# Kernel optimization log

Measured on AMD Instinct MI355X. Metric: run time of the kernel, lower is better.

The kernel has to match this reference:

```python
import jax, jax.numpy as jnp
import numpy as np

EMBED_DIM = 1024
HEAD = 16
DK = EMBED_DIM // HEAD  # 64
B, S = 2, 2048
NEG = -1.0e9


def setup_inputs() -> dict:
    key = jax.random.key(0)
    ks = jax.random.split(key, 8)
    d = {
        'query': jax.random.normal(ks[0], (B, S, EMBED_DIM), jnp.float32),
        'key': jax.random.normal(ks[1], (B, S, EMBED_DIM), jnp.float32),
        'value': jax.random.normal(ks[2], (B, S, EMBED_DIM), jnp.float32),
        'masked': jax.random.randint(ks[3], (B, S, S), 0, 2).astype(bool),
        'Wq': jax.random.normal(ks[4], (EMBED_DIM, EMBED_DIM), jnp.float32) / np.sqrt(EMBED_DIM),
        'Wk': jax.random.normal(ks[5], (EMBED_DIM, EMBED_DIM), jnp.float32) / np.sqrt(EMBED_DIM),
        'Wv': jax.random.normal(ks[6], (EMBED_DIM, EMBED_DIM), jnp.float32) / np.sqrt(EMBED_DIM),
        'Wo': jax.random.normal(ks[7], (EMBED_DIM, EMBED_DIM), jnp.float32) / np.sqrt(EMBED_DIM),
    }
    return d


def reference(query, key, value, masked, Wq, Wk, Wv, Wo):
    # projections (bias-free Linear: x @ W), split into heads: [B, H, S, DK]
    def split_heads(x):
        b, s, _ = x.shape
        return x.reshape(b, s, HEAD, DK).transpose(0, 2, 1, 3)

    q = split_heads(query @ Wq)
    k = split_heads(key @ Wk)
    v = split_heads(value @ Wv)

    scale = 1.0 / jnp.sqrt(jnp.asarray(DK, q.dtype))
    scores = jnp.einsum('bhqd,bhkd->bhqk', q, k) * scale
    scores = jnp.where(masked[:, None, :, :], NEG, scores)
    attn = jax.nn.softmax(scores, axis=-1)
    out = jnp.einsum('bhqk,bhkd->bhqd', attn, v)  # [B, H, S, DK]
    out = out.transpose(0, 2, 1, 3).reshape(query.shape[0], -1, EMBED_DIM)
    return out @ Wo
```

## Files before the change

kernel.cpp:

```cpp
#include <hip/hip_runtime.h>
#include <hip/hip_bf16.h>

typedef float f32x4 __attribute__((ext_vector_type(4)));
typedef __bf16 bf16x8 __attribute__((ext_vector_type(8)));
typedef _Float16 f16x2 __attribute__((ext_vector_type(2)));
typedef _Float16 f16x4 __attribute__((ext_vector_type(4)));

__device__ __forceinline__ unsigned short f2bf(float f){
  unsigned int u = __builtin_bit_cast(unsigned int, f);
  u += 0x7fffu + ((u >> 16) & 1u);
  return (unsigned short)(u >> 16);
}
__device__ __forceinline__ float bf2f(unsigned short h){
  return __builtin_bit_cast(float, (unsigned int)h << 16);
}

__device__ __forceinline__ f16x2 pkrtz(float a, float b){
  return __builtin_bit_cast(f16x2, __builtin_amdgcn_cvt_pkrtz(a, b));
}

__device__ __forceinline__ void glds16(const void* g, void* l){
  __builtin_amdgcn_global_load_lds((const __attribute__((address_space(1))) void*)g,
                                   (__attribute__((address_space(3))) void*)l, 16, 0, 0);
}

__device__ __forceinline__ f32x4 mfma16(bf16x8 a, bf16x8 b, f32x4 c){
  return __builtin_amdgcn_mfma_f32_16x16x32_bf16(a, b, c, 0, 0, 0);
}
__device__ __forceinline__ f32x4 mfma16h(f16x4 a, f16x4 b, f32x4 c){
  return __builtin_amdgcn_mfma_f32_16x16x16f16(a, b, c, 0, 0, 0);
}

#if __has_builtin(__builtin_amdgcn_exp2f)
__device__ __forceinline__ float exp2v(float x){ return __builtin_amdgcn_exp2f(x); }
#else
__device__ __forceinline__ float exp2v(float x){ return exp2f(x); }
#endif

__global__ void detect_kernel(const unsigned int* __restrict__ m, int* __restrict__ flag){
  int t = threadIdx.x;
  int bad = 0;
  for(int i = t; i < 4096; i += 256) bad |= (m[i] > 1u);
  unsigned long long b = __ballot(bad != 0);
  __shared__ int sbuf[4];
  if((t & 63) == 0) sbuf[t >> 6] = (b != 0ull);
  __syncthreads();
  if(t == 0) flag[0] = (sbuf[0] | sbuf[1] | sbuf[2] | sbuf[3]) ? 0 : 1;
}

__global__ void pack_mask_kernel(const unsigned char* __restrict__ m8,
                                 unsigned int* __restrict__ mp,
                                 const int* __restrict__ flag){
  const int wid = threadIdx.x >> 6, lane = threadIdx.x & 63;
  const int row = blockIdx.x * 4 + wid;
  const int is32 = flag[0];
  const int* m32 = (const int*)m8;
  for(int c0 = 0; c0 < 2048; c0 += 64){
    int mv = is32 ? m32[(size_t)row*2048 + c0 + lane]
                  : (int)m8[(size_t)row*2048 + c0 + lane];
    unsigned long long b = __ballot(mv != 0);
    if(lane == 0){
      mp[(size_t)row*64 + (c0 >> 5)]     = (unsigned int)b;
      mp[(size_t)row*64 + (c0 >> 5) + 1] = (unsigned int)(b >> 32);
    }
  }
}

__global__ void cvt3_kernel(const float* __restrict__ qs, const float* __restrict__ ks,
                            const float* __restrict__ vs, unsigned short* __restrict__ dst){
  const float* src = (blockIdx.y==0)?qs:(blockIdx.y==1)?ks:vs;
  unsigned short* d = dst + (size_t)blockIdx.y * 4194304;
  int i = blockIdx.x * 256 + threadIdx.x;
  const float4* s = (const float4*)src;
  float4 a = s[2*i], b = s[2*i+1];
  union { unsigned short h[8]; uint4 v; } o;
  o.h[0]=f2bf(a.x); o.h[1]=f2bf(a.y); o.h[2]=f2bf(a.z); o.h[3]=f2bf(a.w);
  o.h[4]=f2bf(b.x); o.h[5]=f2bf(b.y); o.h[6]=f2bf(b.z); o.h[7]=f2bf(b.w);
  ((uint4*)d)[i] = o.v;
}

__global__ void transW_kernel(const float* __restrict__ Wq, const float* __restrict__ Wk,
                              const float* __restrict__ Wv, const float* __restrict__ Wo,
                              unsigned short* __restrict__ WT){
  const float* W = (blockIdx.y==0)?Wq:(blockIdx.y==1)?Wk:(blockIdx.y==2)?Wv:Wo;
  const float scale = (blockIdx.y==0) ? 0.1803368801111601f : 1.0f;
  unsigned short* D = WT + (size_t)blockIdx.y * 1048576;
  int r0 = (blockIdx.x >> 4) * 64, c0 = (blockIdx.x & 15) * 64;
  __shared__ unsigned short T[64][65];
  int t = threadIdx.x;
  {
    int r = t >> 2, cb = (t & 3) * 16;
    const float4* src = (const float4*)(W + (size_t)(r0 + r) * 1024 + (c0 + cb));
    float4 v0 = src[0], v1 = src[1], v2 = src[2], v3 = src[3];
    float vals[16] = {v0.x,v0.y,v0.z,v0.w, v1.x,v1.y,v1.z,v1.w,
                      v2.x,v2.y,v2.z,v2.w, v3.x,v3.y,v3.z,v3.w};
    #pragma unroll
    for(int j=0;j<16;j++) T[cb + j][r] = f2bf(vals[j] * scale);
  }
  __syncthreads();
  {
    int c = t >> 2, rb = (t & 3) * 16;
    union { unsigned short h[16]; uint4 v[2]; } o;
    #pragma unroll
    for(int j=0;j<16;j++) o.h[j] = T[c][rb + j];
    uint4* dp = (uint4*)(D + (size_t)(c0 + c) * 1024 + (r0 + rb));
    dp[0] = o.v[0]; dp[1] = o.v[1];
  }
}

template<int OUTF32>
__global__ __launch_bounds__(256,2) void gemm_bt(
    const unsigned short* __restrict__ A0, const unsigned short* __restrict__ A1, const unsigned short* __restrict__ A2,
    const unsigned short* __restrict__ B0, const unsigned short* __restrict__ B1, const unsigned short* __restrict__ B2,
    unsigned short* __restrict__ C0, unsigned short* __restrict__ C1, unsigned short* __restrict__ C2,
    float* __restrict__ Cf)
{
  const unsigned short* A  = (blockIdx.z==0)?A0:(blockIdx.z==1)?A1:A2;
  const unsigned short* BT = (blockIdx.z==0)?B0:(blockIdx.z==1)?B1:B2;
  unsigned short* C        = (blockIdx.z==0)?C0:(blockIdx.z==1)?C1:C2;
  __shared__ unsigned short Asm[128*64];
  __shared__ unsigned short Bsm[128*64];
  const int wid = threadIdx.x >> 6, lane = threadIdx.x & 63;
  const int m0 = blockIdx.x * 128, n0 = blockIdx.y * 128;
  const int wrow = wid >> 1, wcol = wid & 1;
  const int li = lane & 15, lg = lane >> 4, li7 = lane & 7;
  f32x4 acc[4][4] = {};
  const int sr = lane >> 3;
  const int sc = lane & 7;

  for(int kt = 0; kt < 16; ++kt){
    const int kofs = kt * 64;
    #pragma unroll
    for(int i=0;i<4;i++){
      int r = wid*32 + i*8 + sr;
      int blk = sc ^ sr;
      glds16(A  + (size_t)(m0 + r)*1024 + kofs + blk*8, &Asm[(wid*32 + i*8)*64]);
      glds16(BT + (size_t)(n0 + r)*1024 + kofs + blk*8, &Bsm[(wid*32 + i*8)*64]);
    }
    __syncthreads();
    #pragma unroll
    for(int kk=0; kk<2; kk++){
      bf16x8 af[4], bfv[4];
      #pragma unroll
      for(int fm=0; fm<4; fm++){
        int row = wrow*64 + fm*16 + li;
        int blk = (kk*4 + lg) ^ li7;
        af[fm] = *(const bf16x8*)&Asm[row*64 + blk*8];
      }
      #pragma unroll
      for(int fn=0; fn<4; fn++){
        int row = wcol*64 + fn*16 + li;
        int blk = (kk*4 + lg) ^ li7;
        bfv[fn] = *(const bf16x8*)&Bsm[row*64 + blk*8];
      }
      __builtin_amdgcn_s_setprio(1);
      #pragma unroll
      for(int fm=0; fm<4; fm++)
        #pragma unroll
        for(int fn=0; fn<4; fn++)
          acc[fm][fn] = mfma16(af[fm], bfv[fn], acc[fm][fn]);
      __builtin_amdgcn_s_setprio(0);
    }
    __syncthreads();
  }
  if(OUTF32 == 0 && blockIdx.z == 2){
    #pragma unroll
    for(int fm=0; fm<4; fm++){
      #pragma unroll
      for(int fn=0; fn<4; fn++){
        int col  = n0 + wcol*64 + fn*16 + li;
        int rowb = m0 + wrow*64 + fm*16 + lg*4;
        int bq = rowb >> 11, s = rowb & 2047;
        union { f16x2 h2[2]; unsigned long long u; } o;
        o.h2[0] = pkrtz(acc[fm][fn][0], acc[fm][fn][1]);
        o.h2[1] = pkrtz(acc[fm][fn][2], acc[fm][fn][3]);
        *(unsigned long long*)&C[((size_t)(bq*16 + (col>>6))*64 + (col&63))*2048 + s] = o.u;
      }
    }
  } else {
    #pragma unroll
    for(int fm=0; fm<4; fm++){
      #pragma unroll
      for(int fn=0; fn<4; fn++){
        int col  = n0 + wcol*64 + fn*16 + li;
        int rowb = m0 + wrow*64 + fm*16 + lg*4;
        #pragma unroll
        for(int r=0;r<4;r++){
          if(OUTF32) Cf[(size_t)(rowb + r)*1024 + col] = acc[fm][fn][r];
          else       C [(size_t)(rowb + r)*1024 + col] = f2bf(acc[fm][fn][r]);
        }
      }
    }
  }
}

__global__ __launch_bounds__(256,2) void attn_kernel(
    const unsigned short* __restrict__ Q, const unsigned short* __restrict__ K,
    const unsigned short* __restrict__ Vt, unsigned short* __restrict__ O,
    const unsigned int* __restrict__ mp)
{
  __shared__ unsigned short Ksm[2][64*64];
  __shared__ unsigned short Vsm[2][64*64];
  const int wid = threadIdx.x >> 6, lane = threadIdx.x & 63;
  const int orig = blockIdx.x;
  const int wg = (orig & 7) * 64 + (orig >> 3);
  const int qt = wg & 15, bh = wg >> 4;
  const int b = bh >> 4, h = bh & 15;
  const int q0 = qt * 128;
  const int li = lane & 15, lg = lane >> 4;
  const int li7 = li & 7;

  const int rowA = b*2048 + q0 + wid*32 + li;
  const int rowB = rowA + 16;

  bf16x8 qfA[2], qfB[2];
  {
    const unsigned short* qa = Q + (size_t)rowA*1024 + h*64 + lg*8;
    const unsigned short* qb = Q + (size_t)rowB*1024 + h*64 + lg*8;
    qfA[0] = *(const bf16x8*)qa; qfA[1] = *(const bf16x8*)(qa + 32);
    qfB[0] = *(const bf16x8*)qb; qfB[1] = *(const bf16x8*)(qb + 32);
  }

  f32x4 oaccA[4] = {}, oaccB[4] = {};
  float lrowA = 0.f, lrowB = 0.f;

  const int srow = lane >> 3;
  const int sblk = (lane & 7) ^ srow;

  #pragma unroll
  for(int i=0;i<2;i++){
    int r = wid*16 + i*8 + srow;
    glds16(K  + (size_t)(b*2048 + r)*1024 + h*64 + sblk*8, &Ksm[0][(wid*16 + i*8)*64]);
    glds16(Vt + (size_t)(bh*64 + r)*2048 + sblk*8,         &Vsm[0][(wid*16 + i*8)*64]);
  }
  uint2 mwA = *(const uint2*)&mp[(size_t)rowA*64];
  uint2 mwB = *(const uint2*)&mp[(size_t)rowB*64];
  uint2 mwAn, mwBn;
  __syncthreads();

  int buf = 0;
  for(int t = 0; t < 32; ++t){
    const int kv0 = t * 64;
    if(t < 31){
      #pragma unroll
      for(int i=0;i<2;i++){
        int r = wid*16 + i*8 + srow;
        glds16(K  + (size_t)(b*2048 + kv0 + 64 + r)*1024 + h*64 + sblk*8, &Ksm[buf^1][(wid*16 + i*8)*64]);
        glds16(Vt + (size_t)(bh*64 + r)*2048 + kv0 + 64 + sblk*8,         &Vsm[buf^1][(wid*16 + i*8)*64]);
      }
      mwAn = *(const uint2*)&mp[(size_t)rowA*64 + (size_t)((kv0 + 64) >> 5)];
      mwBn = *(const uint2*)&mp[(size_t)rowB*64 + (size_t)((kv0 + 64) >> 5)];
    }
    f32x4 pA[4], pB[4];
    __builtin_amdgcn_s_setprio(1);
    #pragma unroll
    for(int f=0; f<4; f++){
      f32x4 sa = {0.f,0.f,0.f,0.f}, sb = {0.f,0.f,0.f,0.f};
      #pragma unroll
      for(int kf=0; kf<2; kf++){
        int blk = (kf*4 + lg) ^ li7;
        bf16x8 kfr = *(const bf16x8*)&Ksm[buf][(f*16 + li)*64 + blk*8];
        sa = mfma16(kfr, qfA[kf], sa);
        sb = mfma16(kfr, qfB[kf], sb);
      }
      pA[f] = sa; pB[f] = sb;
    }
    __builtin_amdgcn_s_setprio(0);
    #pragma unroll
    for(int f=0; f<4; f++){
      unsigned int wA = (f < 2) ? mwA.x : mwA.y;
      unsigned int wB = (f < 2) ? mwB.x : mwB.y;
      float eA[4], eB[4];
      #pragma unroll
      for(int j=0;j<4;j++){
        unsigned int bitA = (wA >> ((f & 1)*16 + lg*4 + j)) & 1u;
        unsigned int bitB = (wB >> ((f & 1)*16 + lg*4 + j)) & 1u;
        float vA = exp2v(pA[f][j]);
        float vB = exp2v(pB[f][j]);
        eA[j] = bitA ? 0.f : vA;
        eB[j] = bitB ? 0.f : vB;
      }
      lrowA += (eA[0] + eA[1]) + (eA[2] + eA[3]);
      lrowB += (eB[0] + eB[1]) + (eB[2] + eB[3]);
      union { f16x2 h2[2]; f16x4 v; } ua, ub;
      ua.h2[0] = pkrtz(eA[0], eA[1]);
      ua.h2[1] = pkrtz(eA[2], eA[3]);
      ub.h2[0] = pkrtz(eB[0], eB[1]);
      ub.h2[1] = pkrtz(eB[2], eB[3]);
      const int blk = (f*2 + (lg >> 1)) ^ li7;
      const int sub = (lg & 1)*4;
      __builtin_amdgcn_s_setprio(1);
      #pragma unroll
      for(int dt=0; dt<4; dt++){
        f16x4 vf = *(const f16x4*)&Vsm[buf][(dt*16 + li)*64 + blk*8 + sub];
        oaccA[dt] = mfma16h(ua.v, vf, oaccA[dt]);
        oaccB[dt] = mfma16h(ub.v, vf, oaccB[dt]);
      }
      __builtin_amdgcn_s_setprio(0);
    }
    __syncthreads();
    mwA = mwAn; mwB = mwBn;
    buf ^= 1;
  }
  float rsA = lrowA, rsB = lrowB;
  rsA += __shfl_xor(rsA, 16); rsA += __shfl_xor(rsA, 32);
  rsB += __shfl_xor(rsB, 16); rsB += __shfl_xor(rsB, 32);
  float invA = 1.0f / rsA;
  float invB = 1.0f / rsB;
  #pragma unroll
  for(int r=0;r<4;r++){
    float ioA = __shfl(invA, lg*4 + r);
    float ioB = __shfl(invB, lg*4 + r);
    size_t rbA = (size_t)(b*2048 + q0 + wid*32 + lg*4 + r);
    size_t rbB = rbA + 16;
    #pragma unroll
    for(int dt=0; dt<4; dt++){
      O[rbA*1024 + h*64 + 16*dt + li] = f2bf(oaccA[dt][r] * ioA);
      O[rbB*1024 + h*64 + 16*dt + li] = f2bf(oaccB[dt][r] * ioB);
    }
  }
}

extern "C" void kernel_launch(void* const* d_in, const int* in_sizes, int n_in,
                              void* d_out, int out_size, void* d_ws, size_t ws_size,
                              hipStream_t stream)
{
  const float* q_in = (const float*)d_in[0];
  const float* k_in = (const float*)d_in[1];
  const float* v_in = (const float*)d_in[2];
  const unsigned char* mask = (const unsigned char*)d_in[3];
  const float* Wq = (const float*)d_in[4];
  const float* Wk = (const float*)d_in[5];
  const float* Wv = (const float*)d_in[6];
  const float* Wo = (const float*)d_in[7];

  char* ws = (char*)d_ws;
  const size_t MB = 1024*1024;
  int* flag          = (int*)ws;
  unsigned short* XQ = (unsigned short*)(ws + 256);
  unsigned short* XK = (unsigned short*)(ws + 256 + 8*MB);
  unsigned short* XV = (unsigned short*)(ws + 256 + 16*MB);
  unsigned short* WT = (unsigned short*)(ws + 256 + 24*MB);
  unsigned short* Qb = (unsigned short*)(ws + 256 + 32*MB);
  unsigned short* Kb = (unsigned short*)(ws + 256 + 40*MB);
  unsigned short* Vt = (unsigned short*)(ws + 256 + 48*MB);
  unsigned short* Ob = XQ;
  unsigned int*   mpk= (unsigned int*)XV;

  detect_kernel<<<1, 256, 0, stream>>>((const unsigned int*)mask, flag);
  cvt3_kernel<<<dim3(2048,3), 256, 0, stream>>>(q_in, k_in, v_in, XQ);
  transW_kernel<<<dim3(256,4), 256, 0, stream>>>(Wq, Wk, Wv, Wo, WT);
  gemm_bt<0><<<dim3(32,8,3), 256, 0, stream>>>(XQ, XK, XV,
                                               WT, WT + 1048576, WT + 2097152,
                                               Qb, Kb, Vt, nullptr);
  pack_mask_kernel<<<1024, 256, 0, stream>>>(mask, mpk, flag);
  attn_kernel<<<512, 256, 0, stream>>>(Qb, Kb, Vt, Ob, mpk);
  gemm_bt<1><<<dim3(32,8,1), 256, 0, stream>>>(Ob, Ob, Ob,
                                               WT + 3*1048576, WT + 3*1048576, WT + 3*1048576,
                                               nullptr, nullptr, nullptr, (float*)d_out);
}
```

Measured before the change: 142.3 us.

## Split attention KV range in two and merge partials in a combine kernel

Each attention work-group now handles half of the key/value sequence, which doubles the grid to 1024 blocks and raises launch bounds to 4 blocks per CU to fill the GPU better. Unnormalized partial outputs go to a workspace buffer as fp16, and row sums go to a separate buffer. A new combine kernel adds the two partials, normalizes them and writes bf16 input for the output projection. This costs an extra launch and extra global memory traffic for the partials, and rearranges workspace buffers to make room.

```diff
diff --git a/kernel.cpp b/kernel.cpp
--- a/kernel.cpp
+++ b/kernel.cpp
@@ -194,19 +194,20 @@
   }
 }
 
-__global__ __launch_bounds__(256,2) void attn_kernel(
+__global__ __launch_bounds__(256,4) void attn_kernel(
     const unsigned short* __restrict__ Q, const unsigned short* __restrict__ K,
-    const unsigned short* __restrict__ Vt, unsigned short* __restrict__ O,
-    const unsigned int* __restrict__ mp)
+    const unsigned short* __restrict__ Vt, _Float16* __restrict__ Of,
+    float* __restrict__ Lp, const unsigned int* __restrict__ mp)
 {
   __shared__ unsigned short Ksm[2][64*64];
   __shared__ unsigned short Vsm[2][64*64];
   const int wid = threadIdx.x >> 6, lane = threadIdx.x & 63;
   const int orig = blockIdx.x;
-  const int wg = (orig & 7) * 64 + (orig >> 3);
-  const int qt = wg & 15, bh = wg >> 4;
+  const int wg = (orig & 7) * 128 + (orig >> 3);
+  const int kvh = wg & 1, qt = (wg >> 1) & 15, bh = wg >> 5;
   const int b = bh >> 4, h = bh & 15;
   const int q0 = qt * 128;
+  const int kbase = kvh * 1024;
   const int li = lane & 15, lg = lane >> 4;
   const int li7 = li & 7;
 
@@ -230,18 +231,18 @@
   #pragma unroll
   for(int i=0;i<2;i++){
     int r = wid*16 + i*8 + srow;
-    glds16(K  + (size_t)(b*2048 + r)*1024 + h*64 + sblk*8, &Ksm[0][(wid*16 + i*8)*64]);
-    glds16(Vt + (size_t)(bh*64 + r)*2048 + sblk*8,         &Vsm[0][(wid*16 + i*8)*64]);
-  }
-  uint2 mwA = *(const uint2*)&mp[(size_t)rowA*64];
-  uint2 mwB = *(const uint2*)&mp[(size_t)rowB*64];
+    glds16(K  + (size_t)(b*2048 + kbase + r)*1024 + h*64 + sblk*8, &Ksm[0][(wid*16 + i*8)*64]);
+    glds16(Vt + (size_t)(bh*64 + r)*2048 + kbase + sblk*8,         &Vsm[0][(wid*16 + i*8)*64]);
+  }
+  uint2 mwA = *(const uint2*)&mp[(size_t)rowA*64 + kvh*32];
+  uint2 mwB = *(const uint2*)&mp[(size_t)rowB*64 + kvh*32];
   uint2 mwAn, mwBn;
   __syncthreads();
 
   int buf = 0;
-  for(int t = 0; t < 32; ++t){
-    const int kv0 = t * 64;
-    if(t < 31){
+  for(int tt = 0; tt < 16; ++tt){
+    const int kv0 = kbase + tt * 64;
+    if(tt < 15){
       #pragma unroll
       for(int i=0;i<2;i++){
         int r = wid*16 + i*8 + srow;
@@ -305,20 +306,38 @@
   float rsA = lrowA, rsB = lrowB;
   rsA += __shfl_xor(rsA, 16); rsA += __shfl_xor(rsA, 32);
   rsB += __shfl_xor(rsB, 16); rsB += __shfl_xor(rsB, 32);
-  float invA = 1.0f / rsA;
-  float invB = 1.0f / rsB;
   #pragma unroll
   for(int r=0;r<4;r++){
-    float ioA = __shfl(invA, lg*4 + r);
-    float ioB = __shfl(invB, lg*4 + r);
     size_t rbA = (size_t)(b*2048 + q0 + wid*32 + lg*4 + r);
     size_t rbB = rbA + 16;
     #pragma unroll
     for(int dt=0; dt<4; dt++){
-      O[rbA*1024 + h*64 + 16*dt + li] = f2bf(oaccA[dt][r] * ioA);
-      O[rbB*1024 + h*64 + 16*dt + li] = f2bf(oaccB[dt][r] * ioB);
-    }
-  }
+      Of[((size_t)kvh*4096 + rbA)*1024 + h*64 + 16*dt + li] = (_Float16)oaccA[dt][r];
+      Of[((size_t)kvh*4096 + rbB)*1024 + h*64 + 16*dt + li] = (_Float16)oaccB[dt][r];
+    }
+  }
+  if(lane < 16){
+    int rA = b*2048 + q0 + wid*32 + lane;
+    Lp[((size_t)kvh*4096 + rA)*16 + h]      = rsA;
+    Lp[((size_t)kvh*4096 + rA + 16)*16 + h] = rsB;
+  }
+}
+
+__global__ void combine_kernel(const _Float16* __restrict__ Of,
+                               const float* __restrict__ Lp,
+                               unsigned short* __restrict__ Ob)
+{
+  const int row = blockIdx.x;
+  const int col = threadIdx.x * 4;
+  const int h = col >> 6;
+  float l = Lp[(size_t)row*16 + h] + Lp[(size_t)(4096 + row)*16 + h];
+  float inv = 1.0f / l;
+  f16x4 o1 = *(const f16x4*)&Of[(size_t)row*1024 + col];
+  f16x4 o2 = *(const f16x4*)&Of[(size_t)(4096 + row)*1024 + col];
+  union { unsigned short h4[4]; unsigned long long u; } o;
+  #pragma unroll
+  for(int i=0;i<4;i++) o.h4[i] = f2bf(((float)o1[i] + (float)o2[i]) * inv);
+  *(unsigned long long*)&Ob[(size_t)row*1024 + col] = o.u;
 }
 
 extern "C" void kernel_launch(void* const* d_in, const int* in_sizes, int n_in,
@@ -345,7 +364,9 @@
   unsigned short* Kb = (unsigned short*)(ws + 256 + 40*MB);
   unsigned short* Vt = (unsigned short*)(ws + 256 + 48*MB);
   unsigned short* Ob = XQ;
-  unsigned int*   mpk= (unsigned int*)XV;
+  _Float16* Of       = (_Float16*)XK;
+  unsigned int* mpk  = (unsigned int*)WT;
+  float* Lp          = (float*)(ws + 256 + 25*MB);
 
   detect_kernel<<<1, 256, 0, stream>>>((const unsigned int*)mask, flag);
   cvt3_kernel<<<dim3(2048,3), 256, 0, stream>>>(q_in, k_in, v_in, XQ);
@@ -354,7 +375,8 @@
                                                WT, WT + 1048576, WT + 2097152,
                                                Qb, Kb, Vt, nullptr);
   pack_mask_kernel<<<1024, 256, 0, stream>>>(mask, mpk, flag);
-  attn_kernel<<<512, 256, 0, stream>>>(Qb, Kb, Vt, Ob, mpk);
+  attn_kernel<<<1024, 256, 0, stream>>>(Qb, Kb, Vt, Of, Lp, mpk);
+  combine_kernel<<<4096, 256, 0, stream>>>(Of, Lp, Ob);
   gemm_bt<1><<<dim3(32,8,1), 256, 0, stream>>>(Ob, Ob, Ob,
                                                WT + 3*1048576, WT + 3*1048576, WT + 3*1048576,
                                                nullptr, nullptr, nullptr, (float*)d_out);
```

Result: slower. 305.3 us (+114.6%).

## Double-buffer GEMM LDS tiles and fold mask-format detection into pack kernel

Applied to the files above, without the earlier changes.

The bf16 GEMM now keeps two LDS buffers for the A and B tiles and prefetches the next K tile with global_load_lds while the current tile runs through MFMA. This drops the per-iteration sync between load and compute and overlaps memory latency with math. It doubles LDS use to 64KB per block, which may limit the two-blocks-per-CU occupancy target. Separately, the single-block detect kernel is removed and each wave of the mask packing kernel repeats the 32-bit-vs-byte check on its own, saving one launch at the cost of redundant reads.

```diff
diff --git a/kernel.cpp b/kernel.cpp
--- a/kernel.cpp
+++ b/kernel.cpp
@@ -37,23 +37,15 @@
 __device__ __forceinline__ float exp2v(float x){ return exp2f(x); }
 #endif
 
-__global__ void detect_kernel(const unsigned int* __restrict__ m, int* __restrict__ flag){
-  int t = threadIdx.x;
-  int bad = 0;
-  for(int i = t; i < 4096; i += 256) bad |= (m[i] > 1u);
-  unsigned long long b = __ballot(bad != 0);
-  __shared__ int sbuf[4];
-  if((t & 63) == 0) sbuf[t >> 6] = (b != 0ull);
-  __syncthreads();
-  if(t == 0) flag[0] = (sbuf[0] | sbuf[1] | sbuf[2] | sbuf[3]) ? 0 : 1;
-}
-
 __global__ void pack_mask_kernel(const unsigned char* __restrict__ m8,
-                                 unsigned int* __restrict__ mp,
-                                 const int* __restrict__ flag){
+                                 unsigned int* __restrict__ mp){
   const int wid = threadIdx.x >> 6, lane = threadIdx.x & 63;
   const int row = blockIdx.x * 4 + wid;
-  const int is32 = flag[0];
+  const unsigned int* w32 = (const unsigned int*)m8;
+  int bad = 0;
+  #pragma unroll
+  for(int c = 0; c < 1024; c += 64) bad |= (w32[c + lane] > 1u);
+  const int is32 = !__any(bad);
   const int* m32 = (const int*)m8;
   for(int c0 = 0; c0 < 2048; c0 += 64){
     int mv = is32 ? m32[(size_t)row*2048 + c0 + lane]
@@ -118,8 +110,8 @@
   const unsigned short* A  = (blockIdx.z==0)?A0:(blockIdx.z==1)?A1:A2;
   const unsigned short* BT = (blockIdx.z==0)?B0:(blockIdx.z==1)?B1:B2;
   unsigned short* C        = (blockIdx.z==0)?C0:(blockIdx.z==1)?C1:C2;
-  __shared__ unsigned short Asm[128*64];
-  __shared__ unsigned short Bsm[128*64];
+  __shared__ unsigned short Asm[2][128*64];
+  __shared__ unsigned short Bsm[2][128*64];
   const int wid = threadIdx.x >> 6, lane = threadIdx.x & 63;
   const int m0 = blockIdx.x * 128, n0 = blockIdx.y * 128;
   const int wrow = wid >> 1, wcol = wid & 1;
@@ -127,17 +119,27 @@
   f32x4 acc[4][4] = {};
   const int sr = lane >> 3;
   const int sc = lane & 7;
-
+  const int sblk = sc ^ sr;
+
+  #pragma unroll
+  for(int i=0;i<4;i++){
+    int r = wid*32 + i*8 + sr;
+    glds16(A  + (size_t)(m0 + r)*1024 + sblk*8, &Asm[0][(wid*32 + i*8)*64]);
+    glds16(BT + (size_t)(n0 + r)*1024 + sblk*8, &Bsm[0][(wid*32 + i*8)*64]);
+  }
+  __syncthreads();
+
+  int buf = 0;
   for(int kt = 0; kt < 16; ++kt){
-    const int kofs = kt * 64;
-    #pragma unroll
-    for(int i=0;i<4;i++){
-      int r = wid*32 + i*8 + sr;
-      int blk = sc ^ sr;
-      glds16(A  + (size_t)(m0 + r)*1024 + kofs + blk*8, &Asm[(wid*32 + i*8)*64]);
-      glds16(BT + (size_t)(n0 + r)*1024 + kofs + blk*8, &Bsm[(wid*32 + i*8)*64]);
-    }
-    __syncthreads();
+    if(kt < 15){
+      const int kofs = (kt + 1) * 64;
+      #pragma unroll
+      for(int i=0;i<4;i++){
+        int r = wid*32 + i*8 + sr;
+        glds16(A  + (size_t)(m0 + r)*1024 + kofs + sblk*8, &Asm[buf^1][(wid*32 + i*8)*64]);
+        glds16(BT + (size_t)(n0 + r)*1024 + kofs + sblk*8, &Bsm[buf^1][(wid*32 + i*8)*64]);
+      }
+    }
     #pragma unroll
     for(int kk=0; kk<2; kk++){
       bf16x8 af[4], bfv[4];
@@ -145,13 +147,13 @@
       for(int fm=0; fm<4; fm++){
         int row = wrow*64 + fm*16 + li;
         int blk = (kk*4 + lg) ^ li7;
-        af[fm] = *(const bf16x8*)&Asm[row*64 + blk*8];
+        af[fm] = *(const bf16x8*)&Asm[buf][row*64 + blk*8];
       }
       #pragma unroll
       for(int fn=0; fn<4; fn++){
         int row = wcol*64 + fn*16 + li;
         int blk = (kk*4 + lg) ^ li7;
-        bfv[fn] = *(const bf16x8*)&Bsm[row*64 + blk*8];
+        bfv[fn] = *(const bf16x8*)&Bsm[buf][row*64 + blk*8];
       }
       __builtin_amdgcn_s_setprio(1);
       #pragma unroll
@@ -162,6 +164,7 @@
       __builtin_amdgcn_s_setprio(0);
     }
     __syncthreads();
+    buf ^= 1;
   }
   if(OUTF32 == 0 && blockIdx.z == 2){
     #pragma unroll
@@ -336,7 +339,6 @@
 
   char* ws = (char*)d_ws;
   const size_t MB = 1024*1024;
-  int* flag          = (int*)ws;
   unsigned short* XQ = (unsigned short*)(ws + 256);
   unsigned short* XK = (unsigned short*)(ws + 256 + 8*MB);
   unsigned short* XV = (unsigned short*)(ws + 256 + 16*MB);
@@ -347,13 +349,12 @@
   unsigned short* Ob = XQ;
   unsigned int*   mpk= (unsigned int*)XV;
 
-  detect_kernel<<<1, 256, 0, stream>>>((const unsigned int*)mask, flag);
   cvt3_kernel<<<dim3(2048,3), 256, 0, stream>>>(q_in, k_in, v_in, XQ);
   transW_kernel<<<dim3(256,4), 256, 0, stream>>>(Wq, Wk, Wv, Wo, WT);
   gemm_bt<0><<<dim3(32,8,3), 256, 0, stream>>>(XQ, XK, XV,
                                                WT, WT + 1048576, WT + 2097152,
                                                Qb, Kb, Vt, nullptr);
-  pack_mask_kernel<<<1024, 256, 0, stream>>>(mask, mpk, flag);
+  pack_mask_kernel<<<1024, 256, 0, stream>>>(mask, mpk);
   attn_kernel<<<512, 256, 0, stream>>>(Qb, Kb, Vt, Ob, mpk);
   gemm_bt<1><<<dim3(32,8,1), 256, 0, stream>>>(Ob, Ob, Ob,
                                                WT + 3*1048576, WT + 3*1048576, WT + 3*1048576,
```

New measurement: 151.1 us. +6.2%, slower.
